# Optimization experiments

Hardware: AMD Instinct MI355X
Metric: run time of the kernel (lower is better)

## Reference

```python
import jax, jax.numpy as jnp
import numpy as np

NEG = -10000.0
SINK = 16  # first 16 keys are always-attended sink tokens


def setup_inputs() -> dict:
    key = jax.random.key(0)
    k0, k1, k2 = jax.random.split(key, 3)
    B, H, KH, S, D = 1, 16, 4, 2048, 128
    return {
        "query": jax.random.normal(k0, (B, H, S, D), dtype=jnp.float32),
        "key_t": jax.random.normal(k1, (B, KH, S, D), dtype=jnp.float32),
        "value": jax.random.normal(k2, (B, KH, S, D), dtype=jnp.float32),
        "lsh_threshold": jnp.full((KH,), 70.0, dtype=jnp.float32),
        "top_k": 64,
        "window_size": 128,
    }


def reference(query, key_t, value, lsh_threshold, top_k, window_size):
    # query: [B,H,S,D]; key_t/value: [B,KH,S,D] (GQA, QH = H//KH)
    B, H, S, D = query.shape
    KH = key_t.shape[1]
    QH = H // KH
    q = query.reshape(B, KH, QH, S, D)

    # LSH sign-bit matching count. packbits64(x>=0) + (D - xor_popcount) ==
    # number of positions where sign(q)==sign(k) == (D + <sgn(q),sgn(k)>)/2.
    qs = jnp.where(q >= 0, 1.0, -1.0).astype(jnp.float32)
    ksgn = jnp.where(key_t >= 0, 1.0, -1.0).astype(jnp.float32)
    match = (D + jnp.einsum('bkqsd,bkld->bkqsl', qs, ksgn)) * 0.5  # [B,KH,QH,S,S]
    # max over the QH group (dim=2, keepdim) then compare against per-KV-head threshold
    lsh_mask = match.max(axis=2, keepdims=True) > lsh_threshold.reshape(1, KH, 1, 1, 1)

    qi = jnp.arange(S)[:, None]
    ki = jnp.arange(S)[None, :]
    causal = qi >= ki                                             # [S,S]
    window = ((jnp.abs(qi - ki) < window_size) | (ki < SINK)) & causal

    mask = causal & lsh_mask                                      # [B,KH,QH,S,S]

    scale = 1.0 / jnp.sqrt(jnp.asarray(D, jnp.float32))
    scores = jnp.einsum('bkqsd,bkld->bkqsl', q, key_t) * scale    # [B,KH,QH,S,S]
    scores = jnp.where(jnp.logical_not(mask) & jnp.logical_not(window), NEG, scores)

    # long-term candidates: exclude the local window, then take top_k per query row
    scores_lt = jnp.where(window, NEG, scores)
    _, idx = jax.lax.top_k(scores_lt, top_k)                      # [B,KH,QH,S,top_k]
    topk_mask = jnp.put_along_axis(
        jnp.zeros(scores.shape, dtype=bool), idx, True, axis=-1, inplace=False)

    both = window | topk_mask
    probs = jax.nn.softmax(jnp.where(both, scores, NEG), axis=-1)
    out = jnp.einsum('bkqsl,bkld->bskqd', probs, value)           # [B,S,KH,QH,D]
    return out.reshape(B, S, H * D)
```

## Files before the change

kernel.cpp:

```cpp
#include <hip/hip_runtime.h>

#define S_LEN   2048
#define D_DIM   128
#define KH_N    4
#define QH_N    4
#define H_N     (KH_N * QH_N)
#define SINK_N  16
#define MAXW    160
#define MAXC    1904
#define MAXT    2048
#define NREG    16
#define CHUNK   1024
#define MAXSEL  208
#define PLANE32 676
#define TIECAP  672

typedef __attribute__((ext_vector_type(8))) _Float16 f16x8;
typedef __attribute__((ext_vector_type(2))) _Float16 f16x2;
typedef __attribute__((ext_vector_type(4))) float f32x4;

__device__ __forceinline__ void lds_fence() {
  asm volatile("s_waitcnt lgkmcnt(0)" ::: "memory");
}
__device__ __forceinline__ unsigned short f2h(float f) {
  _Float16 h = (_Float16)f;
  return __builtin_bit_cast(unsigned short, h);
}
__device__ __forceinline__ unsigned int pkrtz_u32(float a, float b) {
  return __builtin_bit_cast(unsigned int, __builtin_amdgcn_cvt_pkrtz(a, b));
}
__device__ __forceinline__ unsigned int pack_okey16(float a, float b) {
  unsigned int u = pkrtz_u32(a, b);
  unsigned int t = (u >> 15) & 0x00010001u;
  return u ^ ((t * 0x7FFFu) | 0x80008000u);
}
__device__ __forceinline__ float okinv16(unsigned int k) {
  unsigned short bits = (k & 0x8000u) ? (unsigned short)(k & 0x7FFFu)
                                      : (unsigned short)(~k & 0xFFFFu);
  return (float)__builtin_bit_cast(_Float16, bits);
}

__global__ __launch_bounds__(256) void pack_kernel(
    const float* __restrict__ k, const float* __restrict__ v,
    unsigned long long* __restrict__ signs,
    unsigned short* __restrict__ kf16, unsigned int* __restrict__ vf16) {
  const int wid  = (blockIdx.x * 256 + threadIdx.x) >> 6;
  const int lane = threadIdx.x & 63;
  const int rbase = wid * 4;
  const int KROWS = KH_N * S_LEN;

  if (rbase < KROWS) {
    const float* src = k + (size_t)rbase * D_DIM;
    float a[4], b[4];
#pragma unroll
    for (int r = 0; r < 4; r++) {
      a[r] = src[r * D_DIM + lane];
      b[r] = src[r * D_DIM + 64 + lane];
    }
#pragma unroll
    for (int r = 0; r < 4; r++) {
      unsigned long long b0 = __ballot(a[r] >= 0.0f);
      unsigned long long b1 = __ballot(b[r] >= 0.0f);
      if (lane == 0) {
        signs[(size_t)(rbase + r) * 2]     = b0;
        signs[(size_t)(rbase + r) * 2 + 1] = b1;
      }
      unsigned short* rb = kf16 + (size_t)(rbase + r) * 128;
      rb[lane]      = f2h(a[r]);
      rb[64 + lane] = f2h(b[r]);
    }
  } else {
    int vr = rbase - KROWS;
    const float* src = v + (size_t)vr * D_DIM;
    float2 f2[4];
#pragma unroll
    for (int r = 0; r < 4; r++)
      f2[r] = *(const float2*)(src + r * D_DIM + lane * 2);
#pragma unroll
    for (int r = 0; r < 4; r++) {
      unsigned int pk = (unsigned int)f2h(f2[r].x) |
                        ((unsigned int)f2h(f2[r].y) << 16);
      vf16[(size_t)(vr + r) * 64 + lane] = pk;
    }
  }
}

__global__ __launch_bounds__(256, 5) void attn_kernel(
    const float* __restrict__ query, const float* __restrict__ thr,
    const int* __restrict__ p_topk, const int* __restrict__ p_wsz,
    const unsigned long long* __restrict__ signs,
    const unsigned short* __restrict__ kf16,
    const unsigned int* __restrict__ vf16,
    float* __restrict__ out) {
  const int xcd  = blockIdx.x & 7;
  const int kh   = xcd >> 1;
  const int s    = (S_LEN - 1) - (((blockIdx.x >> 3) << 1) | (xcd & 1));
  const int tid  = threadIdx.x;
  const int lane = tid & 63;
  const int qh   = tid >> 6;
  const int col  = lane & 15;
  const int quad = lane >> 4;

  __shared__ __align__(16) unsigned int buf[QH_N * PLANE32];
  __shared__ __align__(16) unsigned short q_f16[QH_N][136];
  __shared__ unsigned short idx_sh[MAXT];
  __shared__ unsigned long long qs_sh[QH_N][2];
  __shared__ int ncand_sh;

  const int   topk   = *p_topk;
  const int   wsz    = *p_wsz;
  const float thresh = thr[kh];
  const float scale  = 0.088388347648318447f;

  {
    int h0 = tid >> 7, d = tid & 127;
    float f0 = query[((size_t)(kh * QH_N + h0) * S_LEN + s) * D_DIM + d];
    float f1 = query[((size_t)(kh * QH_N + h0 + 2) * S_LEN + s) * D_DIM + d];
    unsigned long long b0 = __ballot(f0 >= 0.0f);
    unsigned long long b1 = __ballot(f1 >= 0.0f);
    if (lane == 0) {
      qs_sh[qh >> 1][qh & 1] = b0;
      qs_sh[2 + (qh >> 1)][qh & 1] = b1;
    }
    q_f16[h0][d]     = f2h(f0 * scale);
    q_f16[h0 + 2][d] = f2h(f1 * scale);
  }
  if (tid == 0) ncand_sh = 0;

  int wlo = s - (wsz - 1); if (wlo < 0) wlo = 0;
  int nsink = wlo < SINK_N ? wlo : SINK_N;
  int nw = nsink + (s - wlo + 1);
  if (nw > MAXW) nw = MAXW;
  for (int e = tid; e < nw; e += 256)
    idx_sh[e] = (unsigned short)(e < nsink ? e : wlo + (e - nsink));
  __syncthreads();

  unsigned long long qs0[QH_N], qs1[QH_N];
#pragma unroll
  for (int h = 0; h < QH_N; h++) { qs0[h] = qs_sh[h][0]; qs1[h] = qs_sh[h][1]; }
  const unsigned long long* ksg = signs + (size_t)kh * S_LEN * 2;
  int lt_hi = s - wsz;
  for (int l0 = SINK_N; l0 <= lt_hi; l0 += 512) {
    int la = l0 + tid;
    int lb = la + 256;
    bool ma = false, mb = false;
    if (la <= lt_hi) {
      ulonglong2 kk = *(const ulonglong2*)(ksg + 2 * la);
      int best = 0;
#pragma unroll
      for (int h = 0; h < QH_N; h++) {
        int m = 128 - __popcll(qs0[h] ^ kk.x) - __popcll(qs1[h] ^ kk.y);
        best = best > m ? best : m;
      }
      ma = ((float)best > thresh);
    }
    if (lb <= lt_hi) {
      ulonglong2 kk = *(const ulonglong2*)(ksg + 2 * lb);
      int best = 0;
#pragma unroll
      for (int h = 0; h < QH_N; h++) {
        int m = 128 - __popcll(qs0[h] ^ kk.x) - __popcll(qs1[h] ^ kk.y);
        best = best > m ? best : m;
      }
      mb = ((float)best > thresh);
    }
    unsigned long long m1 = __ballot(ma);
    unsigned long long m2 = __ballot(mb);
    if (m1 | m2) {
      int pc1 = __popcll(m1);
      int base = 0;
      if (lane == 0) base = atomicAdd(&ncand_sh, pc1 + __popcll(m2));
      base = __shfl(base, 0);
      if (ma) {
        int pos = base + __popcll(m1 & ((1ull << lane) - 1ull));
        if (pos < MAXC) idx_sh[nw + pos] = (unsigned short)la;
      }
      if (mb) {
        int pos = base + pc1 + __popcll(m2 & ((1ull << lane) - 1ull));
        if (pos < MAXC) idx_sh[nw + pos] = (unsigned short)lb;
      }
    }
  }
  __syncthreads();
  int nc = ncand_sh < MAXC ? ncand_sh : MAXC;
  int ntot = nw + nc;
  int ntot_pad = (ntot + 15) & ~15;
  for (int i = ntot + tid; i < ntot_pad; i += 256) idx_sh[i] = 0;
  __syncthreads();

  f16x8 bfrag[4];
  f16x8 bzero = {0, 0, 0, 0, 0, 0, 0, 0};
#pragma unroll
  for (int ks = 0; ks < 4; ks++)
    bfrag[ks] = (col < 4) ? *(const f16x8*)&q_f16[col][ks * 32 + quad * 8] : bzero;

  const unsigned short* kf_h = kf16 + ((size_t)kh << 11) * 128;
  unsigned int creg[NREG];
#pragma unroll
  for (int i = 0; i < NREG; i++) creg[i] = 0u;

  for (int cb = 0; cb < 2; cb++) {
    int cbase = cb * CHUNK;
    int chunk_n = ntot_pad - cbase;
    if (chunk_n <= 0) break;
    if (chunk_n > CHUNK) chunk_n = CHUNK;
    int ntiles = chunk_n >> 4;
    for (int t = qh; t < ntiles; t += QH_N) {
      int tb = cbase + t * 16;
      int krow = idx_sh[tb + col];
      const unsigned char* ab =
          (const unsigned char*)(kf_h + (size_t)krow * 128) + quad * 16;
      f16x8 a0 = *(const f16x8*)(ab + 0);
      f16x8 a1 = *(const f16x8*)(ab + 64);
      f16x8 a2 = *(const f16x8*)(ab + 128);
      f16x8 a3 = *(const f16x8*)(ab + 192);
      f32x4 acc = {0.f, 0.f, 0.f, 0.f};
      acc = __builtin_amdgcn_mfma_f32_16x16x32_f16(a0, bfrag[0], acc, 0, 0, 0);
      acc = __builtin_amdgcn_mfma_f32_16x16x32_f16(a1, bfrag[1], acc, 0, 0, 0);
      acc = __builtin_amdgcn_mfma_f32_16x16x32_f16(a2, bfrag[2], acc, 0, 0, 0);
      acc = __builtin_amdgcn_mfma_f32_16x16x32_f16(a3, bfrag[3], acc, 0, 0, 0);
      if (col < 4) {
        unsigned int k01 = pack_okey16(acc[0], acc[1]);
        unsigned int k23 = pack_okey16(acc[2], acc[3]);
        int off = ((tb - cbase) >> 1) + quad * 2;
        buf[col * PLANE32 + off]     = k01;
        buf[col * PLANE32 + off + 1] = k23;
      }
    }
    __syncthreads();
#pragma unroll
    for (int j = 0; j < 8; j++) {
      int m = j * 64 + lane;
      if (2 * m < chunk_n) creg[cb * 8 + j] = buf[qh * PLANE32 + m];
    }
    __syncthreads();
  }
  const int imax = (ntot + 127) >> 7;

  unsigned int*       histw = &buf[qh * PLANE32];
  unsigned long long* selq  = (unsigned long long*)&buf[qh * PLANE32 + 256];

  unsigned int mx16 = 0;
#pragma unroll
  for (int i = 0; i < NREG; i++) {
    if (i >= imax) break;
    unsigned int u = creg[i];
    int e0 = i * 128 + 2 * lane;
    unsigned int h0 = u & 0xFFFFu, h1 = u >> 16;
    if (e0 < ntot && h0 > mx16) mx16 = h0;
    if (e0 + 1 < ntot && h1 > mx16) mx16 = h1;
  }
#pragma unroll
  for (int off = 32; off > 0; off >>= 1) {
    unsigned int t = __shfl_down(mx16, off);
    mx16 = t > mx16 ? t : mx16;
  }
  mx16 = __shfl(mx16, 0);
  const float mxf = okinv16(mx16);

  bool selAll = (nc <= topk);
  unsigned int tkey = 0;
  bool useTie = false;
  int l_cut = S_LEN;
  if (!selAll) {
    unsigned int prefix = 0;
    int want = topk;
    unsigned int ceq = 0;
    for (int pass = 0; pass < 2; pass++) {
      int sh = 8 - pass * 8;
      {
        uint4 z = {0u, 0u, 0u, 0u};
        *(uint4*)&histw[lane * 4] = z;
      }
      lds_fence();
#pragma unroll
      for (int i = 0; i < NREG; i++) {
        if (i >= imax) break;
        unsigned int u = creg[i];
        int e0 = i * 128 + 2 * lane;
#pragma unroll
        for (int h = 0; h < 2; h++) {
          int e = e0 + h;
          if (e >= nw && e < ntot) {
            unsigned int key = h ? (u >> 16) : (u & 0xFFFFu);
            bool match = (pass == 0) || ((key >> 8) == prefix);
            if (match) atomicAdd(&histw[(key >> sh) & 255u], 1u);
          }
        }
      }
      lds_fence();
      uint4 cc = *(const uint4*)&histw[lane * 4];
      unsigned int c0 = cc.x, c1 = cc.y, c2 = cc.z, c3 = cc.w;
      unsigned int S3 = c3, S2 = c2 + S3, S1 = c1 + S2, S0 = c0 + S1;
      unsigned int tot = S0;
      unsigned int suf = tot;
#pragma unroll
      for (int off = 1; off < 64; off <<= 1) {
        unsigned int t = __shfl_down(suf, off);
        if (lane + off < 64) suf += t;
      }
      unsigned long long mk = __ballot(suf >= (unsigned int)want);
      int L = 63 - __clzll(mk);
      unsigned int se = suf - tot;
      unsigned int s3 = S3 + se, s2 = S2 + se, s1 = S1 + se, s0 = S0 + se;
      int j; unsigned int above, csel;
      unsigned int w = (unsigned int)want;
      if (s3 >= w)      { j = 3; above = s3 - c3; csel = c3; }
      else if (s2 >= w) { j = 2; above = s2 - c2; csel = c2; }
      else if (s1 >= w) { j = 1; above = s1 - c1; csel = c1; }
      else              { j = 0; above = s0 - c0; csel = c0; }
      int d_me = (lane << 2) | j;
      int wp_me = want - (int)above;
      int digit = __shfl(d_me, L);
      want = __shfl(wp_me, L);
      ceq = (unsigned int)__shfl((int)csel, L);
      prefix = (prefix << 8) | (unsigned int)digit;
    }
    tkey = prefix;
    int rem = want;
    if ((int)ceq > rem) {
      useTie = true;
      if ((int)ceq <= TIECAP) {
        unsigned int* tls = histw;
        int tb = 0;
#pragma unroll
        for (int i = 0; i < NREG; i++) {
          if (i >= imax) break;
          unsigned int u = creg[i];
          int e0 = i * 128 + 2 * lane;
#pragma unroll
          for (int h = 0; h < 2; h++) {
            int e = e0 + h;
            bool tied = false;
            if (e >= nw && e < ntot) {
              unsigned int key = h ? (u >> 16) : (u & 0xFFFFu);
              tied = (key == tkey);
            }
            unsigned long long m = __ballot(tied);
            if (tied) {
              int pos = tb + __popcll(m & ((1ull << lane) - 1ull));
              tls[pos] = (unsigned int)idx_sh[e];
            }
            tb += (int)__popcll(m);
          }
        }
        lds_fence();
        unsigned int lcut = (unsigned int)S_LEN;
        for (int i = lane; i < (int)ceq; i += 64) {
          unsigned int v = tls[i];
          int rank = 0;
          for (int j2 = 0; j2 < (int)ceq; j2++) rank += (tls[j2] < v);
          if (rank == rem - 1) lcut = v;
        }
#pragma unroll
        for (int off = 32; off > 0; off >>= 1) {
          unsigned int t = __shfl_down(lcut, off);
          lcut = t < lcut ? t : lcut;
        }
        l_cut = (int)__shfl((int)lcut, 0);
      } else {
        int lo = SINK_N, hi = lt_hi;
        while (lo < hi) {
          int mid = (lo + hi) >> 1;
          int cn = 0;
#pragma unroll
          for (int i = 0; i < NREG; i++) {
            if (i >= imax) break;
            unsigned int u = creg[i];
            int e0 = i * 128 + 2 * lane;
#pragma unroll
            for (int h = 0; h < 2; h++) {
              int e = e0 + h;
              if (e >= nw && e < ntot) {
                unsigned int key = h ? (u >> 16) : (u & 0xFFFFu);
                cn += (key == tkey && (int)idx_sh[e] <= mid);
              }
            }
          }
#pragma unroll
          for (int off = 32; off > 0; off >>= 1) cn += __shfl_down(cn, off);
          cn = __shfl(cn, 0);
          if (cn >= rem) hi = mid; else lo = mid + 1;
        }
        l_cut = lo;
      }
    }
  }

  float sum = 0.0f;
  int bse = 0;
#pragma unroll
  for (int i = 0; i < NREG; i++) {
    if (i >= imax) break;
    unsigned int u = creg[i];
    int e0 = i * 128 + 2 * lane;
#pragma unroll
    for (int h = 0; h < 2; h++) {
      int e = e0 + h;
      bool act = false;
      float p = 0.f;
      if (e < ntot) {
        unsigned int key = h ? (u >> 16) : (u & 0xFFFFu);
        bool inc = (e < nw) || selAll;
        if (!inc)
          inc = (key > tkey) ||
                (key == tkey && (!useTie || (int)idx_sh[e] <= l_cut));
        if (inc) { act = true; p = __expf(okinv16(key) - mxf); sum += p; }
      }
      unsigned long long m = __ballot(act);
      if (act) {
        int pi = bse + __popcll(m & ((1ull << lane) - 1ull));
        selq[pi] = ((unsigned long long)idx_sh[e] << 32) |
                   (unsigned long long)__float_as_uint(p);
      }
      bse += (int)__popcll(m);
    }
  }
#pragma unroll
  for (int off = 32; off > 0; off >>= 1) sum += __shfl_down(sum, off);
  sum = __shfl(sum, 0);
  float rinv = 1.0f / sum;

  int nsel = bse;
  int nsel16 = (nsel + 15) & ~15;
  if (lane < nsel16 - nsel) selq[nsel + lane] = 0ull;
  lds_fence();

  const int sub = lane & 15;
  const int quarter = lane >> 4;
  float av[8] = {0.f, 0.f, 0.f, 0.f, 0.f, 0.f, 0.f, 0.f};
  const uint4* vb4 = (const uint4*)(vf16 + ((size_t)kh << 11) * 64);
  for (int e = 0; e < nsel16; e += 16) {
    const unsigned long long* sq = &selq[e + 4 * quarter];
    ulonglong2 spA = *(const ulonglong2*)(sq);
    ulonglong2 spB = *(const ulonglong2*)(sq + 2);
    int l0 = (int)(spA.x >> 32), l1 = (int)(spA.y >> 32);
    int l2 = (int)(spB.x >> 32), l3 = (int)(spB.y >> 32);
    uint4 v0 = vb4[(size_t)l0 * 16 + sub];
    uint4 v1 = vb4[(size_t)l1 * 16 + sub];
    uint4 v2 = vb4[(size_t)l2 * 16 + sub];
    uint4 v3 = vb4[(size_t)l3 * 16 + sub];
    f16x2 phA = __builtin_bit_cast(
        f16x2, pkrtz_u32(__uint_as_float((unsigned int)spA.x),
                         __uint_as_float((unsigned int)spA.y)));
    f16x2 phB = __builtin_bit_cast(
        f16x2, pkrtz_u32(__uint_as_float((unsigned int)spB.x),
                         __uint_as_float((unsigned int)spB.y)));
#define DOT2P(va, vb, ph, comp, i0, i1)                                       \
    {                                                                         \
      unsigned int lo_ = __builtin_amdgcn_perm(vb.comp, va.comp, 0x05040100u); \
      unsigned int hi_ = __builtin_amdgcn_perm(vb.comp, va.comp, 0x07060302u); \
      av[i0] = __builtin_amdgcn_fdot2(__builtin_bit_cast(f16x2, lo_), ph,     \
                                      av[i0], false);                         \
      av[i1] = __builtin_amdgcn_fdot2(__builtin_bit_cast(f16x2, hi_), ph,     \
                                      av[i1], false);                         \
    }
    DOT2P(v0, v1, phA, x, 0, 1) DOT2P(v0, v1, phA, y, 2, 3)
    DOT2P(v0, v1, phA, z, 4, 5) DOT2P(v0, v1, phA, w, 6, 7)
    DOT2P(v2, v3, phB, x, 0, 1) DOT2P(v2, v3, phB, y, 2, 3)
    DOT2P(v2, v3, phB, z, 4, 5) DOT2P(v2, v3, phB, w, 6, 7)
#undef DOT2P
  }
#pragma unroll
  for (int d = 0; d < 8; d++) {
    av[d] += __shfl_xor(av[d], 16);
    av[d] += __shfl_xor(av[d], 32);
  }
  if (lane < 16) {
    size_t o = (size_t)s * (H_N * D_DIM) + (size_t)(kh * QH_N + qh) * D_DIM
             + (size_t)sub * 8;
    f32x4 r0 = {av[0] * rinv, av[1] * rinv, av[2] * rinv, av[3] * rinv};
    f32x4 r1 = {av[4] * rinv, av[5] * rinv, av[6] * rinv, av[7] * rinv};
    __builtin_nontemporal_store(r0, (f32x4*)(out + o));
    __builtin_nontemporal_store(r1, (f32x4*)(out + o + 4));
  }
}

extern "C" void kernel_launch(void* const* d_in, const int* in_sizes, int n_in,
                              void* d_out, int out_size, void* d_ws, size_t ws_size,
                              hipStream_t stream) {
  const float* query = (const float*)d_in[0];
  const float* key   = (const float*)d_in[1];
  const float* value = (const float*)d_in[2];
  const float* thr   = (const float*)d_in[3];
  const int* p_topk  = (const int*)d_in[4];
  const int* p_wsz   = (const int*)d_in[5];
  float* out = (float*)d_out;

  char* ws = (char*)d_ws;
  unsigned long long* signs = (unsigned long long*)ws;
  unsigned short* kf16 = (unsigned short*)(ws + (size_t)KH_N * S_LEN * 16);
  unsigned int* vf16 = (unsigned int*)(ws + (size_t)KH_N * S_LEN * 16
                                          + (size_t)KH_N * S_LEN * 256);

  pack_kernel<<<1024, 256, 0, stream>>>(key, value, signs, kf16, vf16);

  attn_kernel<<<KH_N * S_LEN, 256, 0, stream>>>(
      query, thr, p_topk, p_wsz, signs, kf16, vf16, out);
}
```

Measured before the change: 252.0 us.

## Score all causal keys densely and track LSH candidates with a bitmask

Replaces the compacted index list of window plus LSH candidates with a per-row bitmask in shared memory. QK scores are then computed for every causal key row in order rather than through gathered rows. The change removes the atomic compaction, the index-list indirection and the gather loads, but performs more MFMA work when candidates are sparse. Window and candidate membership are recomputed from positions and mask bits during the top-k and softmax stages.

```diff
diff --git a/kernel.cpp b/kernel.cpp
--- a/kernel.cpp
+++ b/kernel.cpp
@@ -6,12 +6,8 @@
 #define QH_N    4
 #define H_N     (KH_N * QH_N)
 #define SINK_N  16
-#define MAXW    160
-#define MAXC    1904
-#define MAXT    2048
 #define NREG    16
 #define CHUNK   1024
-#define MAXSEL  208
 #define PLANE32 676
 #define TIECAP  672
 
@@ -103,7 +99,7 @@
 
   __shared__ __align__(16) unsigned int buf[QH_N * PLANE32];
   __shared__ __align__(16) unsigned short q_f16[QH_N][136];
-  __shared__ unsigned short idx_sh[MAXT];
+  __shared__ unsigned long long mask_sh[32];
   __shared__ unsigned long long qs_sh[QH_N][2];
   __shared__ int ncand_sh;
 
@@ -125,68 +121,41 @@
     q_f16[h0][d]     = f2h(f0 * scale);
     q_f16[h0 + 2][d] = f2h(f1 * scale);
   }
+  if (tid < 32) mask_sh[tid] = 0ull;
   if (tid == 0) ncand_sh = 0;
-
-  int wlo = s - (wsz - 1); if (wlo < 0) wlo = 0;
-  int nsink = wlo < SINK_N ? wlo : SINK_N;
-  int nw = nsink + (s - wlo + 1);
-  if (nw > MAXW) nw = MAXW;
-  for (int e = tid; e < nw; e += 256)
-    idx_sh[e] = (unsigned short)(e < nsink ? e : wlo + (e - nsink));
   __syncthreads();
 
-  unsigned long long qs0[QH_N], qs1[QH_N];
-#pragma unroll
-  for (int h = 0; h < QH_N; h++) { qs0[h] = qs_sh[h][0]; qs1[h] = qs_sh[h][1]; }
-  const unsigned long long* ksg = signs + (size_t)kh * S_LEN * 2;
-  int lt_hi = s - wsz;
-  for (int l0 = SINK_N; l0 <= lt_hi; l0 += 512) {
-    int la = l0 + tid;
-    int lb = la + 256;
-    bool ma = false, mb = false;
-    if (la <= lt_hi) {
-      ulonglong2 kk = *(const ulonglong2*)(ksg + 2 * la);
-      int best = 0;
-#pragma unroll
-      for (int h = 0; h < QH_N; h++) {
-        int m = 128 - __popcll(qs0[h] ^ kk.x) - __popcll(qs1[h] ^ kk.y);
-        best = best > m ? best : m;
-      }
-      ma = ((float)best > thresh);
-    }
-    if (lb <= lt_hi) {
-      ulonglong2 kk = *(const ulonglong2*)(ksg + 2 * lb);
-      int best = 0;
-#pragma unroll
-      for (int h = 0; h < QH_N; h++) {
-        int m = 128 - __popcll(qs0[h] ^ kk.x) - __popcll(qs1[h] ^ kk.y);
-        best = best > m ? best : m;
-      }
-      mb = ((float)best > thresh);
-    }
-    unsigned long long m1 = __ballot(ma);
-    unsigned long long m2 = __ballot(mb);
-    if (m1 | m2) {
-      int pc1 = __popcll(m1);
-      int base = 0;
-      if (lane == 0) base = atomicAdd(&ncand_sh, pc1 + __popcll(m2));
-      base = __shfl(base, 0);
-      if (ma) {
-        int pos = base + __popcll(m1 & ((1ull << lane) - 1ull));
-        if (pos < MAXC) idx_sh[nw + pos] = (unsigned short)la;
-      }
-      if (mb) {
-        int pos = base + pc1 + __popcll(m2 & ((1ull << lane) - 1ull));
-        if (pos < MAXC) idx_sh[nw + pos] = (unsigned short)lb;
-      }
-    }
+  const int wlo   = (s - (wsz - 1)) > 0 ? (s - (wsz - 1)) : 0;
+  const int lt_hi = s - wsz;
+  const int nrows = s + 1;
+
+  {
+    unsigned long long qs0[QH_N], qs1[QH_N];
+#pragma unroll
+    for (int h = 0; h < QH_N; h++) { qs0[h] = qs_sh[h][0]; qs1[h] = qs_sh[h][1]; }
+    const unsigned long long* ksg = signs + (size_t)kh * S_LEN * 2;
+    int cnt = 0;
+    for (int l0 = 0; l0 <= lt_hi; l0 += 256) {
+      int l = l0 + tid;
+      bool match = false;
+      if (l >= SINK_N && l <= lt_hi) {
+        ulonglong2 kk = *(const ulonglong2*)(ksg + 2 * l);
+        int best = 0;
+#pragma unroll
+        for (int h = 0; h < QH_N; h++) {
+          int m = 128 - __popcll(qs0[h] ^ kk.x) - __popcll(qs1[h] ^ kk.y);
+          best = best > m ? best : m;
+        }
+        match = ((float)best > thresh);
+      }
+      unsigned long long m = __ballot(match);
+      if (lane == 0) mask_sh[(l0 >> 6) + qh] = m;
+      cnt += (int)__popcll(m);
+    }
+    if (lane == 0 && cnt) atomicAdd(&ncand_sh, cnt);
   }
   __syncthreads();
-  int nc = ncand_sh < MAXC ? ncand_sh : MAXC;
-  int ntot = nw + nc;
-  int ntot_pad = (ntot + 15) & ~15;
-  for (int i = ntot + tid; i < ntot_pad; i += 256) idx_sh[i] = 0;
-  __syncthreads();
+  const int nc = ncand_sh;
 
   f16x8 bfrag[4];
   f16x8 bzero = {0, 0, 0, 0, 0, 0, 0, 0};
@@ -199,17 +168,17 @@
 #pragma unroll
   for (int i = 0; i < NREG; i++) creg[i] = 0u;
 
+  int nrows_pad = (nrows + 15) & ~15;
   for (int cb = 0; cb < 2; cb++) {
     int cbase = cb * CHUNK;
-    int chunk_n = ntot_pad - cbase;
+    int chunk_n = nrows_pad - cbase;
     if (chunk_n <= 0) break;
     if (chunk_n > CHUNK) chunk_n = CHUNK;
     int ntiles = chunk_n >> 4;
     for (int t = qh; t < ntiles; t += QH_N) {
       int tb = cbase + t * 16;
-      int krow = idx_sh[tb + col];
       const unsigned char* ab =
-          (const unsigned char*)(kf_h + (size_t)krow * 128) + quad * 16;
+          (const unsigned char*)(kf_h + (size_t)(tb + col) * 128) + quad * 16;
       f16x8 a0 = *(const f16x8*)(ab + 0);
       f16x8 a1 = *(const f16x8*)(ab + 64);
       f16x8 a2 = *(const f16x8*)(ab + 128);
@@ -235,7 +204,15 @@
     }
     __syncthreads();
   }
-  const int imax = (ntot + 127) >> 7;
+  const int imax = (nrows + 127) >> 7;
+
+  unsigned int mybits = 0;
+#pragma unroll
+  for (int i = 0; i < NREG; i++) {
+    if (i >= imax) break;
+    unsigned long long w = mask_sh[2 * i + (lane >> 5)];
+    mybits |= ((unsigned int)((w >> ((2 * lane) & 63)) & 3ull)) << (2 * i);
+  }
 
   unsigned int*       histw = &buf[qh * PLANE32];
   unsigned long long* selq  = (unsigned long long*)&buf[qh * PLANE32 + 256];
@@ -247,8 +224,8 @@
     unsigned int u = creg[i];
     int e0 = i * 128 + 2 * lane;
     unsigned int h0 = u & 0xFFFFu, h1 = u >> 16;
-    if (e0 < ntot && h0 > mx16) mx16 = h0;
-    if (e0 + 1 < ntot && h1 > mx16) mx16 = h1;
+    if (e0 < nrows && h0 > mx16) mx16 = h0;
+    if (e0 + 1 < nrows && h1 > mx16) mx16 = h1;
   }
 #pragma unroll
   for (int off = 32; off > 0; off >>= 1) {
@@ -277,15 +254,16 @@
       for (int i = 0; i < NREG; i++) {
         if (i >= imax) break;
         unsigned int u = creg[i];
-        int e0 = i * 128 + 2 * lane;
-#pragma unroll
-        for (int h = 0; h < 2; h++) {
-          int e = e0 + h;
-          if (e >= nw && e < ntot) {
-            unsigned int key = h ? (u >> 16) : (u & 0xFFFFu);
-            bool match = (pass == 0) || ((key >> 8) == prefix);
-            if (match) atomicAdd(&histw[(key >> sh) & 255u], 1u);
-          }
+        unsigned int b2 = (mybits >> (2 * i)) & 3u;
+        if (b2 & 1u) {
+          unsigned int key = u & 0xFFFFu;
+          if ((pass == 0) || ((key >> 8) == prefix))
+            atomicAdd(&histw[(key >> sh) & 255u], 1u);
+        }
+        if (b2 & 2u) {
+          unsigned int key = u >> 16;
+          if ((pass == 0) || ((key >> 8) == prefix))
+            atomicAdd(&histw[(key >> sh) & 255u], 1u);
         }
       }
       lds_fence();
@@ -327,19 +305,19 @@
         for (int i = 0; i < NREG; i++) {
           if (i >= imax) break;
           unsigned int u = creg[i];
+          unsigned int b2 = (mybits >> (2 * i)) & 3u;
           int e0 = i * 128 + 2 * lane;
 #pragma unroll
           for (int h = 0; h < 2; h++) {
-            int e = e0 + h;
             bool tied = false;
-            if (e >= nw && e < ntot) {
+            if (b2 & (1u << h)) {
               unsigned int key = h ? (u >> 16) : (u & 0xFFFFu);
               tied = (key == tkey);
             }
             unsigned long long m = __ballot(tied);
             if (tied) {
               int pos = tb + __popcll(m & ((1ull << lane) - 1ull));
-              tls[pos] = (unsigned int)idx_sh[e];
+              tls[pos] = (unsigned int)(e0 + h);
             }
             tb += (int)__popcll(m);
           }
@@ -367,13 +345,13 @@
           for (int i = 0; i < NREG; i++) {
             if (i >= imax) break;
             unsigned int u = creg[i];
+            unsigned int b2 = (mybits >> (2 * i)) & 3u;
             int e0 = i * 128 + 2 * lane;
 #pragma unroll
             for (int h = 0; h < 2; h++) {
-              int e = e0 + h;
-              if (e >= nw && e < ntot) {
+              if (b2 & (1u << h)) {
                 unsigned int key = h ? (u >> 16) : (u & 0xFFFFu);
-                cn += (key == tkey && (int)idx_sh[e] <= mid);
+                cn += (key == tkey && (e0 + h) <= mid);
               }
             }
           }
@@ -399,18 +377,19 @@
       int e = e0 + h;
       bool act = false;
       float p = 0.f;
-      if (e < ntot) {
+      if (e < nrows) {
         unsigned int key = h ? (u >> 16) : (u & 0xFFFFu);
-        bool inc = (e < nw) || selAll;
-        if (!inc)
-          inc = (key > tkey) ||
-                (key == tkey && (!useTie || (int)idx_sh[e] <= l_cut));
+        bool win = (e < SINK_N) || (e >= wlo);
+        bool inc = win;
+        if (!inc && ((mybits >> (2 * i + h)) & 1u))
+          inc = selAll || (key > tkey) ||
+                (key == tkey && (!useTie || e <= l_cut));
         if (inc) { act = true; p = __expf(okinv16(key) - mxf); sum += p; }
       }
       unsigned long long m = __ballot(act);
       if (act) {
         int pi = bse + __popcll(m & ((1ull << lane) - 1ull));
-        selq[pi] = ((unsigned long long)idx_sh[e] << 32) |
+        selq[pi] = ((unsigned long long)e << 32) |
                    (unsigned long long)__float_as_uint(p);
       }
       bse += (int)__popcll(m);
```

After: 359.7 us. 1.43x slower.
